# Kernel tuning notes

Measured on AMD Instinct MI355X. Metric: run time of the kernel, lower is better.

The kernel has to match this reference:

```python
import jax, jax.numpy as jnp
import numpy as np
from jax import lax

B, L, D, H = 2, 4096, 1024, 16
K = 4            # short conv kernel size
HD = D // H      # head dim = 64
EPS = 1e-5


def causal_dw_conv(x, w):
    # depthwise causal conv: x [B,L,D], w [D,K]
    xp = jnp.pad(x, ((0, 0), (K - 1, 0), (0, 0)))
    out = xp[:, 0:L, :] * w[:, 0]
    for j in range(1, K):
        out = out + xp[:, j:j + L, :] * w[:, j]
    return out


def setup_inputs() -> dict:
    key = jax.random.key(0)
    ks = jax.random.split(key, 10)
    s = 0.02
    return {
        "hidden_states": jax.random.normal(ks[0], (B, L, D), jnp.float32),
        "Wq": jax.random.normal(ks[1], (D, D), jnp.float32) * s,
        "Wk": jax.random.normal(ks[2], (D, D), jnp.float32) * s,
        "Wv": jax.random.normal(ks[3], (D, D), jnp.float32) * s,
        "Wb": jax.random.normal(ks[4], (D, H), jnp.float32) * s,
        "conv_q": jax.random.normal(ks[5], (D, K), jnp.float32) * s,
        "conv_k": jax.random.normal(ks[6], (D, K), jnp.float32) * s,
        "conv_v": jax.random.normal(ks[7], (D, K), jnp.float32) * s,
        "o_norm_w": jnp.ones((HD,), jnp.float32),
        "Wo": jax.random.normal(ks[8], (D, D), jnp.float32) * s,
    }


def reference(hidden_states, Wq, Wk, Wv, Wb, conv_q, conv_k, conv_v, o_norm_w, Wo):
    x = hidden_states
    # projections + short causal conv with SiLU (qk_activation == 'silu')
    q = jax.nn.silu(causal_dw_conv(x @ Wq, conv_q))
    k = jax.nn.silu(causal_dw_conv(x @ Wk, conv_k))
    v = jax.nn.silu(causal_dw_conv(x @ Wv, conv_v))

    # [B,L,D] -> [L,B,H,hd] for the time scan
    def to_heads(t):
        return t.reshape(B, L, H, HD).transpose(1, 0, 2, 3)

    q, k, v = to_heads(q), to_heads(k), to_heads(v)

    # l2 qk-norm
    q = q / jnp.linalg.norm(q, axis=-1, keepdims=True)
    k = k / jnp.linalg.norm(k, axis=-1, keepdims=True)

    # beta gate [L,B,H]
    beta = jax.nn.sigmoid(x @ Wb).transpose(1, 0, 2)

    def step(S, inp):
        qt, kt, vt, bt = inp  # [B,H,hd] x3, [B,H]
        v_old = jnp.einsum('bhk,bhkv->bhv', kt, S)
        delta = (vt - v_old) * bt[..., None]
        S = S + jnp.einsum('bhk,bhv->bhkv', kt, delta)
        ot = jnp.einsum('bhk,bhkv->bhv', qt, S)
        return S, ot

    S0 = jnp.zeros((B, H, HD, HD), x.dtype)
    _, o = lax.scan(step, S0, (q, k, v, beta))  # o: [L,B,H,hd]
    o = o.transpose(1, 0, 2, 3)  # [B,L,H,hd]

    # per-head RMSNorm
    rms = jax.lax.rsqrt(jnp.mean(o * o, axis=-1, keepdims=True) + EPS)
    o = o * rms * o_norm_w

    return o.reshape(B, L, D) @ Wo
```

## Files before the change

kernel.cpp:

```cpp
#include <hip/hip_runtime.h>
#include <hip/hip_bf16.h>
#include <math.h>

#define BB 2
#define LL 4096
#define DD 1024
#define HH 16
#define HDIM 64
#define CC 64
#define NC 64
#define BH 32
#define GG 8
#define GS 8

typedef __attribute__((ext_vector_type(8))) short short8;
typedef __attribute__((ext_vector_type(4))) float f32x4;
typedef unsigned short u16;
typedef unsigned int u32;

__device__ __forceinline__ u16 f2bf(float f) {
    unsigned int u = __float_as_uint(f);
    unsigned int r = (u + 0x7fffu + ((u >> 16) & 1u)) >> 16;
    return (u16)r;
}
__device__ __forceinline__ float bf2f(u16 h) {
    return __uint_as_float((unsigned)h << 16);
}
__device__ __forceinline__ void split2(float x, u16& h, u16& l) {
    h = f2bf(x);
    l = f2bf(x - bf2f(h));
}
__device__ __forceinline__ u32 packhl(float x) {
    u16 h, l; split2(x, h, l);
    return (u32)h | ((u32)l << 16);
}
__device__ __forceinline__ float unpackhl(u32 v) {
    return bf2f((u16)v) + bf2f((u16)(v >> 16));
}
__device__ __forceinline__ float4 ld_bf4(const u16* p) {
    uint2 v = *(const uint2*)p;
    return make_float4(bf2f((u16)v.x), bf2f((u16)(v.x >> 16)),
                       bf2f((u16)v.y), bf2f((u16)(v.y >> 16)));
}

__device__ __forceinline__ void gld_lds16(const void* g, void* l) {
    __builtin_amdgcn_global_load_lds(
        (const __attribute__((address_space(1))) void*)g,
        (__attribute__((address_space(3))) void*)l, 16, 0, 0);
}

__device__ __forceinline__ int swz(int r, int c) {
    return (r << 6) + ((((c >> 2) ^ (r >> 2)) & 15) << 2) + (c & 3);
}
__device__ __forceinline__ int swze(int r, int c) {
    return (r << 6) + (c ^ (((r ^ (r >> 3)) & 7) << 3));
}

__device__ __forceinline__ void mm64(const u16* __restrict__ Ah, const u16* __restrict__ Al,
                                     const u16* __restrict__ Bh, const u16* __restrict__ Bl,
                                     f32x4* acc, int w, int lane) {
    const int ln = lane & 15, kg = (lane >> 4) * 8;
#pragma unroll
    for (int kb = 0; kb < 2; ++kb) {
        const int k0 = kb * 32 + kg;
        short8 ah = *(const short8*)&Ah[swze(w * 16 + ln, k0)];
        short8 al = *(const short8*)&Al[swze(w * 16 + ln, k0)];
#pragma unroll
        for (int j = 0; j < 4; ++j) {
            short8 bh = *(const short8*)&Bh[swze(j * 16 + ln, k0)];
            short8 bl = *(const short8*)&Bl[swze(j * 16 + ln, k0)];
            acc[j] = __builtin_amdgcn_mfma_f32_16x16x32_bf16(ah, bh, acc[j], 0, 0, 0);
            acc[j] = __builtin_amdgcn_mfma_f32_16x16x32_bf16(ah, bl, acc[j], 0, 0, 0);
            acc[j] = __builtin_amdgcn_mfma_f32_16x16x32_bf16(al, bh, acc[j], 0, 0, 0);
        }
    }
}
__device__ __forceinline__ void mm64_bb(const u16* __restrict__ Ah,
                                        const u16* __restrict__ Bh,
                                        f32x4* acc, int w, int lane) {
    const int ln = lane & 15, kg = (lane >> 4) * 8;
#pragma unroll
    for (int kb = 0; kb < 2; ++kb) {
        const int k0 = kb * 32 + kg;
        short8 ah = *(const short8*)&Ah[swze(w * 16 + ln, k0)];
#pragma unroll
        for (int j = 0; j < 4; ++j) {
            short8 bh = *(const short8*)&Bh[swze(j * 16 + ln, k0)];
            acc[j] = __builtin_amdgcn_mfma_f32_16x16x32_bf16(ah, bh, acc[j], 0, 0, 0);
        }
    }
}
__device__ __forceinline__ void mm64_ab(const u16* __restrict__ Ah,
                                        const u16* __restrict__ Bh, const u16* __restrict__ Bl,
                                        f32x4* acc, int w, int lane) {
    const int ln = lane & 15, kg = (lane >> 4) * 8;
#pragma unroll
    for (int kb = 0; kb < 2; ++kb) {
        const int k0 = kb * 32 + kg;
        short8 ah = *(const short8*)&Ah[swze(w * 16 + ln, k0)];
#pragma unroll
        for (int j = 0; j < 4; ++j) {
            short8 bh = *(const short8*)&Bh[swze(j * 16 + ln, k0)];
            short8 bl = *(const short8*)&Bl[swze(j * 16 + ln, k0)];
            acc[j] = __builtin_amdgcn_mfma_f32_16x16x32_bf16(ah, bh, acc[j], 0, 0, 0);
            acc[j] = __builtin_amdgcn_mfma_f32_16x16x32_bf16(ah, bl, acc[j], 0, 0, 0);
        }
    }
}

__device__ __forceinline__ void g_to_ls(const float* __restrict__ G, u16* Ah, u16* Al, int tid) {
#pragma unroll
    for (int p = 0; p < 4; ++p) {
        int flat = p * 1024 + tid * 4;
        int r = flat >> 6, c = flat & 63;
        float4 v = *(const float4*)&G[flat];
        u16 h0, l0, h1, l1, h2, l2, h3, l3;
        split2(v.x, h0, l0); split2(v.y, h1, l1);
        split2(v.z, h2, l2); split2(v.w, h3, l3);
        int idx = swze(r, c);
        uint2 hv, lv;
        hv.x = (unsigned)h0 | ((unsigned)h1 << 16); hv.y = (unsigned)h2 | ((unsigned)h3 << 16);
        lv.x = (unsigned)l0 | ((unsigned)l1 << 16); lv.y = (unsigned)l2 | ((unsigned)l3 << 16);
        *(uint2*)&Ah[idx] = hv;
        *(uint2*)&Al[idx] = lv;
    }
}
__device__ __forceinline__ void g_to_ls_b(const u16* __restrict__ G16, u16* Ah, int tid) {
#pragma unroll
    for (int p = 0; p < 2; ++p) {
        int flat = p * 2048 + tid * 8;
        int r = flat >> 6, c = flat & 63;
        *(short8*)&Ah[swze(r, c)] = *(const short8*)&G16[flat];
    }
}

__device__ __forceinline__ void pload(uint4 pf[4], const u32* __restrict__ G, int tid) {
    pf[0] = *(const uint4*)&G[tid * 8];
    pf[1] = *(const uint4*)&G[tid * 8 + 4];
    pf[2] = *(const uint4*)&G[2048 + tid * 8];
    pf[3] = *(const uint4*)&G[2048 + tid * 8 + 4];
}
__device__ __forceinline__ void pstore_ls(const uint4 pf[4], u16* Ah, u16* Al, int tid) {
#pragma unroll
    for (int p = 0; p < 2; ++p) {
        int flat = p * 2048 + tid * 8;
        int r = flat >> 6, c = flat & 63;
        uint4 a = pf[2 * p], b = pf[2 * p + 1];
        short8 hi, lo;
        hi[0] = (short)(u16)a.x; hi[1] = (short)(u16)a.y;
        hi[2] = (short)(u16)a.z; hi[3] = (short)(u16)a.w;
        hi[4] = (short)(u16)b.x; hi[5] = (short)(u16)b.y;
        hi[6] = (short)(u16)b.z; hi[7] = (short)(u16)b.w;
        lo[0] = (short)(a.x >> 16); lo[1] = (short)(a.y >> 16);
        lo[2] = (short)(a.z >> 16); lo[3] = (short)(a.w >> 16);
        lo[4] = (short)(b.x >> 16); lo[5] = (short)(b.y >> 16);
        lo[6] = (short)(b.z >> 16); lo[7] = (short)(b.w >> 16);
        *(short8*)&Ah[swze(r, c)] = hi;
        *(short8*)&Al[swze(r, c)] = lo;
    }
}
__device__ __forceinline__ void gp_to_ls(const u32* __restrict__ G, u16* Ah, u16* Al, int tid) {
    uint4 pf[4];
    pload(pf, G, tid);
    pstore_ls(pf, Ah, Al, tid);
}

__device__ __forceinline__ void frag_to_ls(const f32x4* acc, u16* Ah, u16* Al, int w, int lane) {
    const int g = lane >> 4, ln = lane & 15;
#pragma unroll
    for (int j = 0; j < 4; ++j)
#pragma unroll
        for (int r = 0; r < 4; ++r) {
            int row = w * 16 + g * 4 + r, col = j * 16 + ln;
            u16 h, l; split2(acc[j][r], h, l);
            Ah[swze(row, col)] = h;
            Al[swze(row, col)] = l;
        }
}

__device__ __forceinline__ void gp_to_frag(const u32* __restrict__ G, f32x4* acc, int w, int lane) {
    const int g = lane >> 4, ln = lane & 15;
#pragma unroll
    for (int j = 0; j < 4; ++j)
#pragma unroll
        for (int r = 0; r < 4; ++r)
            acc[j][r] = unpackhl(G[(w * 16 + g * 4 + r) * 64 + j * 16 + ln]);
}
__device__ __forceinline__ void gp_add_frag(const u32* __restrict__ G, f32x4* acc, int w, int lane) {
    const int g = lane >> 4, ln = lane & 15;
#pragma unroll
    for (int j = 0; j < 4; ++j)
#pragma unroll
        for (int r = 0; r < 4; ++r)
            acc[j][r] += unpackhl(G[(w * 16 + g * 4 + r) * 64 + j * 16 + ln]);
}
__device__ __forceinline__ void frag_to_gp(const f32x4* acc, u32* __restrict__ G, int w, int lane) {
    const int g = lane >> 4, ln = lane & 15;
#pragma unroll
    for (int j = 0; j < 4; ++j)
#pragma unroll
        for (int r = 0; r < 4; ++r)
            G[(w * 16 + g * 4 + r) * 64 + j * 16 + ln] = packhl(acc[j][r]);
}

__global__ __launch_bounds__(256) void cast_bf16_k(const float* __restrict__ in,
                                                   u16* __restrict__ out) {
    int i = (blockIdx.x * 256 + threadIdx.x) * 8;
    float4 a = *(const float4*)&in[i];
    float4 b = *(const float4*)&in[i + 4];
    uint4 o;
    o.x = (unsigned)f2bf(a.x) | ((unsigned)f2bf(a.y) << 16);
    o.y = (unsigned)f2bf(a.z) | ((unsigned)f2bf(a.w) << 16);
    o.z = (unsigned)f2bf(b.x) | ((unsigned)f2bf(b.y) << 16);
    o.w = (unsigned)f2bf(b.z) | ((unsigned)f2bf(b.w) << 16);
    *(uint4*)&out[i] = o;
}

__global__ __launch_bounds__(256) void transW4_k(const float* __restrict__ W0,
                                                 const float* __restrict__ W1,
                                                 const float* __restrict__ W2,
                                                 const float* __restrict__ W3,
                                                 u16* __restrict__ WT0) {
    __shared__ float t[32][33];
    const int which = blockIdx.z;
    const float* W = (which == 0) ? W0 : (which == 1) ? W1 : (which == 2) ? W2 : W3;
    u16* WT = WT0 + (size_t)which * 1048576;
    const int bx = blockIdx.x * 32, by = blockIdx.y * 32;
#pragma unroll
    for (int p = 0; p < 4; ++p) {
        int idx = p * 256 + threadIdx.x;
        int r = idx >> 5, cc = idx & 31;
        t[r][cc] = W[(size_t)(by + r) * 1024 + bx + cc];
    }
    __syncthreads();
#pragma unroll
    for (int p = 0; p < 4; ++p) {
        int idx = p * 256 + threadIdx.x;
        int r = idx >> 5, cc = idx & 31;
        WT[(size_t)(bx + r) * 1024 + by + cc] = f2bf(t[cc][r]);
    }
}

__device__ __forceinline__ void gemm_core(const u16* A, const u16* BT,
                                          int m0, int n0, f32x4 acc[4][4]) {
    __shared__ __align__(16) short As[3][128 * 32];
    __shared__ __align__(16) short Bs[3][128 * 32];
    const int tid = threadIdx.x;
    const int lane = tid & 63, w = tid >> 6;
    const int wr = w >> 1, wc = w & 1;
    const int ln15 = lane & 15;
    const int erow = tid >> 2;
    const int ecol = (((tid & 3) ^ ((erow >> 1) & 3)) << 3);
    const int kch = lane >> 4;

#define STAGE(buf, k0)                                                        \
    {                                                                         \
        _Pragma("unroll")                                                     \
        for (int r = 0; r < 2; ++r) {                                         \
            gld_lds16(A  + (size_t)(m0 + erow + r * 64) * 1024 + (k0) + ecol, \
                      (short*)As[buf] + r * 2048 + tid * 8);                  \
            gld_lds16(BT + (size_t)(n0 + erow + r * 64) * 1024 + (k0) + ecol, \
                      (short*)Bs[buf] + r * 2048 + tid * 8);                  \
        }                                                                     \
    }

#define COMPUTE(buf)                                                           \
    {                                                                          \
        short8 af[4], bf[4];                                                   \
        _Pragma("unroll")                                                      \
        for (int i = 0; i < 4; ++i) {                                          \
            int row = wr * 64 + i * 16 + ln15;                                 \
            af[i] = *(const short8*)&As[buf][row * 32 + ((kch ^ ((row >> 1) & 3)) << 3)]; \
        }                                                                      \
        _Pragma("unroll")                                                      \
        for (int j = 0; j < 4; ++j) {                                          \
            int row = wc * 64 + j * 16 + ln15;                                 \
            bf[j] = *(const short8*)&Bs[buf][row * 32 + ((kch ^ ((row >> 1) & 3)) << 3)]; \
        }                                                                      \
        __builtin_amdgcn_s_setprio(1);                                         \
        _Pragma("unroll")                                                      \
        for (int i = 0; i < 4; ++i)                                            \
            _Pragma("unroll")                                                  \
            for (int j = 0; j < 4; ++j)                                        \
                acc[i][j] = __builtin_amdgcn_mfma_f32_16x16x32_bf16(af[i], bf[j], acc[i][j], 0, 0, 0); \
        __builtin_amdgcn_s_setprio(0);                                         \
    }

    STAGE(0, 0);
    STAGE(1, 32);
    for (int t = 0; t < 30; ++t) {
        STAGE((t + 2) % 3, (t + 2) * 32);
        asm volatile("s_waitcnt vmcnt(8)" ::: "memory");
        __builtin_amdgcn_sched_barrier(0);
        __builtin_amdgcn_s_barrier();
        COMPUTE(t % 3);
        asm volatile("s_waitcnt lgkmcnt(0)" ::: "memory");
        __builtin_amdgcn_sched_barrier(0);
        __builtin_amdgcn_s_barrier();
    }
    asm volatile("s_waitcnt vmcnt(4)" ::: "memory");
    __builtin_amdgcn_sched_barrier(0);
    __builtin_amdgcn_s_barrier();
    COMPUTE(0);
    asm volatile("s_waitcnt vmcnt(0)" ::: "memory");
    __builtin_amdgcn_sched_barrier(0);
    __builtin_amdgcn_s_barrier();
    COMPUTE(1);
#undef STAGE
#undef COMPUTE
}

__global__ __launch_bounds__(256) void gemm_bf16(const u16* __restrict__ A,
                                                 const u16* __restrict__ BT,
                                                 float* __restrict__ C) {
    const int m0 = blockIdx.y * 128, n0 = blockIdx.x * 128;
    f32x4 acc[4][4] = {};
    gemm_core(A, BT, m0, n0, acc);
    const int lane = threadIdx.x & 63, w = threadIdx.x >> 6;
    const int crow0 = m0 + (w >> 1) * 64 + (lane >> 4) * 4;
    const int ccol0 = n0 + (w & 1) * 64 + (lane & 15);
#pragma unroll
    for (int i = 0; i < 4; ++i)
#pragma unroll
        for (int j = 0; j < 4; ++j)
#pragma unroll
            for (int r = 0; r < 4; ++r)
                C[(size_t)(crow0 + i * 16 + r) * 1024 + ccol0 + j * 16] = acc[i][j][r];
}

__global__ __launch_bounds__(256) void gemm_qkv(const u16* __restrict__ A,
                                                const u16* __restrict__ WT0,
                                                u16* __restrict__ xq16,
                                                u16* __restrict__ xk16,
                                                float* __restrict__ xv) {
    const int which = blockIdx.x >> 3;
    const int n0 = (blockIdx.x & 7) * 128;
    const int m0 = blockIdx.y * 128;
    const u16* BT = WT0 + (size_t)which * 1048576;
    f32x4 acc[4][4] = {};
    gemm_core(A, BT, m0, n0, acc);
    const int lane = threadIdx.x & 63, w = threadIdx.x >> 6;
    const int crow0 = m0 + (w >> 1) * 64 + (lane >> 4) * 4;
    const int ccol0 = n0 + (w & 1) * 64 + (lane & 15);
    if (which == 2) {
#pragma unroll
        for (int i = 0; i < 4; ++i)
#pragma unroll
            for (int j = 0; j < 4; ++j)
#pragma unroll
                for (int r = 0; r < 4; ++r)
                    xv[(size_t)(crow0 + i * 16 + r) * 1024 + ccol0 + j * 16] = acc[i][j][r];
    } else {
        u16* C16 = (which == 0) ? xq16 : xk16;
#pragma unroll
        for (int i = 0; i < 4; ++i)
#pragma unroll
            for (int j = 0; j < 4; ++j)
#pragma unroll
                for (int r = 0; r < 4; ++r)
                    C16[(size_t)(crow0 + i * 16 + r) * 1024 + ccol0 + j * 16] = f2bf(acc[i][j][r]);
    }
}

__global__ __launch_bounds__(256) void beta_k(const float* __restrict__ X,
                                              const float* __restrict__ Wb,
                                              float* __restrict__ beta) {
    int idx = blockIdx.x * 256 + threadIdx.x;
    int row = idx >> 4, h = idx & 15;
    const float* xr = X + (size_t)row * DD;
    float s = 0.f;
    for (int k4 = 0; k4 < DD; k4 += 4) {
        float4 xv = *(const float4*)&xr[k4];
        s += xv.x * Wb[(k4 + 0) * HH + h];
        s += xv.y * Wb[(k4 + 1) * HH + h];
        s += xv.z * Wb[(k4 + 2) * HH + h];
        s += xv.w * Wb[(k4 + 3) * HH + h];
    }
    float bv = 1.f / (1.f + expf(-s));
    int b = row >> 12, l = row & (LL - 1);
    beta[((size_t)b * HH + h) * LL + l] = bv;
}

__global__ __launch_bounds__(256) void conv3_k(const u16* __restrict__ xq16,
                                               const u16* __restrict__ xk16,
                                               const float* __restrict__ xv,
                                               const float* __restrict__ cwq,
                                               const float* __restrict__ cwk,
                                               const float* __restrict__ cwv,
                                               u16* __restrict__ q16,
                                               u16* __restrict__ k16,
                                               float* __restrict__ vout) {
    const int which = blockIdx.z;
    const float* cw = (which == 0) ? cwq : (which == 1) ? cwk : cwv;
    const int l0 = blockIdx.x * 16, b = blockIdx.y;
    const int tid = threadIdx.x;
    const int d0 = tid * 4;
    const float4 w0 = *(const float4*)&cw[(d0 + 0) * 4];
    const float4 w1 = *(const float4*)&cw[(d0 + 1) * 4];
    const float4 w2 = *(const float4*)&cw[(d0 + 2) * 4];
    const float4 w3 = *(const float4*)&cw[(d0 + 3) * 4];
    const int h = d0 >> 6, hd = d0 & 63;
    if (which < 2) {
        const u16* Xb = ((which == 0) ? xq16 : xk16) + (size_t)b * LL * DD;
        u16* O16 = (which == 0) ? q16 : k16;
        float4 xm3 = make_float4(0, 0, 0, 0), xm2 = xm3, xm1 = xm3;
        if (l0 > 0) {
            xm3 = ld_bf4(&Xb[(size_t)(l0 - 3) * DD + d0]);
            xm2 = ld_bf4(&Xb[(size_t)(l0 - 2) * DD + d0]);
            xm1 = ld_bf4(&Xb[(size_t)(l0 - 1) * DD + d0]);
        }
#pragma unroll
        for (int t = 0; t < 16; ++t) {
            const int l = l0 + t;
            float4 xc = ld_bf4(&Xb[(size_t)l * DD + d0]);
            float a0 = xm3.x * w0.x + xm2.x * w0.y + xm1.x * w0.z + xc.x * w0.w;
            float a1 = xm3.y * w1.x + xm2.y * w1.y + xm1.y * w1.z + xc.y * w1.w;
            float a2 = xm3.z * w2.x + xm2.z * w2.y + xm1.z * w2.z + xc.z * w2.w;
            float a3 = xm3.w * w3.x + xm2.w * w3.y + xm1.w * w3.z + xc.w * w3.w;
            a0 = a0 / (1.f + expf(-a0));
            a1 = a1 / (1.f + expf(-a1));
            a2 = a2 / (1.f + expf(-a2));
            a3 = a3 / (1.f + expf(-a3));
            float s = a0 * a0 + a1 * a1 + a2 * a2 + a3 * a3;
            s += __shfl_xor(s, 1);
            s += __shfl_xor(s, 2);
            s += __shfl_xor(s, 4);
            s += __shfl_xor(s, 8);
            float sc = rsqrtf(s);
            a0 *= sc; a1 *= sc; a2 *= sc; a3 *= sc;
            uint2 o;
            o.x = (unsigned)f2bf(a0) | ((unsigned)f2bf(a1) << 16);
            o.y = (unsigned)f2bf(a2) | ((unsigned)f2bf(a3) << 16);
            *(uint2*)&O16[(((size_t)b * HH + h) * LL + l) * 64 + hd] = o;
            xm3 = xm2; xm2 = xm1; xm1 = xc;
        }
    } else {
        const float* Xb = xv + (size_t)b * LL * DD;
        float4 xm3 = make_float4(0, 0, 0, 0), xm2 = xm3, xm1 = xm3;
        if (l0 > 0) {
            xm3 = *(const float4*)&Xb[(size_t)(l0 - 3) * DD + d0];
            xm2 = *(const float4*)&Xb[(size_t)(l0 - 2) * DD + d0];
            xm1 = *(const float4*)&Xb[(size_t)(l0 - 1) * DD + d0];
        }
#pragma unroll
        for (int t = 0; t < 16; ++t) {
            const int l = l0 + t;
            float4 xc = *(const float4*)&Xb[(size_t)l * DD + d0];
            float a0 = xm3.x * w0.x + xm2.x * w0.y + xm1.x * w0.z + xc.x * w0.w;
            float a1 = xm3.y * w1.x + xm2.y * w1.y + xm1.y * w1.z + xc.y * w1.w;
            float a2 = xm3.z * w2.x + xm2.z * w2.y + xm1.z * w2.z + xc.z * w2.w;
            float a3 = xm3.w * w3.x + xm2.w * w3.y + xm1.w * w3.z + xc.w * w3.w;
            a0 = a0 / (1.f + expf(-a0));
            a1 = a1 / (1.f + expf(-a1));
            a2 = a2 / (1.f + expf(-a2));
            a3 = a3 / (1.f + expf(-a3));
            *(float4*)&vout[(((size_t)b * HH + h) * LL + l) * 64 + hd] =
                make_float4(a0, a1, a2, a3);
            xm3 = xm2; xm2 = xm1; xm1 = xc;
        }
    }
}

__global__ __launch_bounds__(256) void phaseA6(const u16* __restrict__ kg16,
                                               const float* __restrict__ vg,
                                               const float* __restrict__ betag,
                                               u32* __restrict__ WgP,
                                               u32* __restrict__ UgTP,
                                               u32* __restrict__ PallP,
                                               u32* __restrict__ BallTP) {
    __shared__ __align__(16) char pool[73728];
    u16* Kh   = (u16*)pool;
    u16* KTh  = (u16*)(pool + 8192);
    float* At = (float*)(pool + 16384);
    float* WU = (float*)(pool + 32768);
    u16* WTh  = (u16*)pool;
    u16* WTl  = (u16*)(pool + 16384);
    u16* UTh  = (u16*)(pool + 24576);
    u16* UTl  = (u16*)(pool + 65536);
    float* scr = (float*)(pool + 32768);

    const int c = blockIdx.x, bh = blockIdx.y;
    const int tid = threadIdx.x, lane = tid & 63, w = tid >> 6;
    const int g = lane >> 4, ln = lane & 15;
    const int t0 = (tid >> 4) * 4, d4 = (tid & 15) * 4;
    const size_t base = ((size_t)bh * LL + (size_t)c * 64) * 64;
    const size_t obase = ((size_t)bh * NC + c) * 4096;
    const float* bet = betag + (size_t)bh * LL + (size_t)c * 64;

    g_to_ls_b(kg16 + base, Kh, tid);
    {
        u16 kv[4][4];
#pragma unroll
        for (int i = 0; i < 4; ++i) {
            uint2 v = *(const uint2*)&kg16[base + (size_t)(t0 + i) * 64 + d4];
            kv[i][0] = (u16)v.x; kv[i][1] = (u16)(v.x >> 16);
            kv[i][2] = (u16)v.y; kv[i][3] = (u16)(v.y >> 16);
        }
#pragma unroll
        for (int j = 0; j < 4; ++j) {
            uint2 hv;
            hv.x = (unsigned)kv[0][j] | ((unsigned)kv[1][j] << 16);
            hv.y = (unsigned)kv[2][j] | ((unsigned)kv[3][j] << 16);
            *(uint2*)&KTh[swze(d4 + j, t0)] = hv;
        }
    }
    __syncthreads();
    {
        f32x4 acc[4] = {};
        mm64_bb(Kh, Kh, acc, w, lane);
#pragma unroll
        for (int r = 0; r < 4; ++r) {
            int t = w * 16 + g * 4 + r;
            float bt = bet[t];
#pragma unroll
            for (int j = 0; j < 4; ++j) {
                int s = j * 16 + ln;
                At[t * 64 + s] = (s < t) ? bt * acc[j][r] : 0.f;
            }
        }
    }
#pragma unroll
    for (int p = 0; p < 8; ++p) {
        int flat = p * 1024 + tid * 4;
        int t = flat >> 7, j = flat & 127;
        float bt = bet[t];
        float4 src;
        if (j < 64) src = ld_bf4(&Kh[swze(t, j)]);
        else        src = *(const float4*)&vg[base + (size_t)t * 64 + (j - 64)];
        src.x *= bt; src.y *= bt; src.z *= bt; src.w *= bt;
        *(float4*)&WU[t * 128 + j] = src;
    }
    __syncthreads();
#pragma unroll
    for (int pb = 0; pb < 4; ++pb) {
        const int r0 = pb * 16;
        if (pb > 0) {
            const int col = tid & 127;
            const int rbase = r0 + (tid >> 7) * 8;
            float acc8[8] = {};
            for (int r = 0; r < r0; r += 4) {
                float u0 = WU[(r + 0) * 128 + col], u1 = WU[(r + 1) * 128 + col];
                float u2 = WU[(r + 2) * 128 + col], u3 = WU[(r + 3) * 128 + col];
#pragma unroll
                for (int i = 0; i < 8; ++i) {
                    float4 a4 = *(const float4*)&At[(rbase + i) * 64 + r];
                    acc8[i] += a4.x * u0 + a4.y * u1 + a4.z * u2 + a4.w * u3;
                }
            }
#pragma unroll
            for (int i = 0; i < 8; ++i) WU[(rbase + i) * 128 + col] -= acc8[i];
            __syncthreads();
        }
        if (tid < 128) {
            const int col = tid;
            float wv[16];
            wv[0] = WU[r0 * 128 + col];
#pragma unroll
            for (int t = 1; t < 16; ++t) {
                float a = WU[(r0 + t) * 128 + col];
#pragma unroll
                for (int r = 0; r < t; ++r) a -= At[(r0 + t) * 64 + r0 + r] * wv[r];
                wv[t] = a;
            }
#pragma unroll
            for (int t = 1; t < 16; ++t) WU[(r0 + t) * 128 + col] = wv[t];
        }
        __syncthreads();
    }
#pragma unroll
    for (int p = 0; p < 4; ++p) {
        int flat = p * 1024 + tid * 4;
        int t = flat >> 6, j = flat & 63;
        float4 v = *(const float4*)&WU[t * 128 + j];
        uint4 o;
        o.x = packhl(v.x); o.y = packhl(v.y); o.z = packhl(v.z); o.w = packhl(v.w);
        *(uint4*)&WgP[obase + flat] = o;
    }
    {
        u16 h4[4][4], l4[4][4];
#pragma unroll
        for (int i = 0; i < 4; ++i) {
            float4 v = *(const float4*)&WU[(t0 + i) * 128 + d4];
            split2(v.x, h4[i][0], l4[i][0]); split2(v.y, h4[i][1], l4[i][1]);
            split2(v.z, h4[i][2], l4[i][2]); split2(v.w, h4[i][3], l4[i][3]);
        }
#pragma unroll
        for (int j = 0; j < 4; ++j) {
            uint2 hv, lv;
            hv.x = (unsigned)h4[0][j] | ((unsigned)h4[1][j] << 16);
            hv.y = (unsigned)h4[2][j] | ((unsigned)h4[3][j] << 16);
            lv.x = (unsigned)l4[0][j] | ((unsigned)l4[1][j] << 16);
            lv.y = (unsigned)l4[2][j] | ((unsigned)l4[3][j] << 16);
            *(uint2*)&WTh[swze(d4 + j, t0)] = hv;
            *(uint2*)&WTl[swze(d4 + j, t0)] = lv;
        }
#pragma unroll
        for (int i = 0; i < 4; ++i) {
            float4 v = *(const float4*)&WU[(t0 + i) * 128 + 64 + d4];
            split2(v.x, h4[i][0], l4[i][0]); split2(v.y, h4[i][1], l4[i][1]);
            split2(v.z, h4[i][2], l4[i][2]); split2(v.w, h4[i][3], l4[i][3]);
        }
#pragma unroll
        for (int j = 0; j < 4; ++j) {
            uint2 hv, lv;
            hv.x = (unsigned)h4[0][j] | ((unsigned)h4[1][j] << 16);
            hv.y = (unsigned)h4[2][j] | ((unsigned)h4[3][j] << 16);
            lv.x = (unsigned)l4[0][j] | ((unsigned)l4[1][j] << 16);
            lv.y = (unsigned)l4[2][j] | ((unsigned)l4[3][j] << 16);
            *(uint2*)&UTh[swze(d4 + j, t0)] = hv;
            *(uint2*)&UTl[swze(d4 + j, t0)] = lv;
        }
    }
    __syncthreads();
#pragma unroll
    for (int p = 0; p < 4; ++p) {
        int flat = p * 1024 + tid * 4;
        int n = flat >> 6, tt = flat & 63;
        int idx = swze(n, tt);
        uint2 hh = *(const uint2*)&UTh[idx];
        uint2 ll2 = *(const uint2*)&UTl[idx];
        uint4 o;
        o.x = (hh.x & 0xffffu) | (ll2.x << 16);
        o.y = (hh.x >> 16) | (ll2.x & 0xffff0000u);
        o.z = (hh.y & 0xffffu) | (ll2.y << 16);
        o.w = (hh.y >> 16) | (ll2.y & 0xffff0000u);
        *(uint4*)&UgTP[obase + flat] = o;
    }
    f32x4 aP[4] = {}, aB[4] = {};
    mm64_ab(KTh, WTh, WTl, aP, w, lane);
    mm64_ab(KTh, UTh, UTl, aB, w, lane);
#pragma unroll
    for (int j = 0; j < 4; ++j)
#pragma unroll
        for (int r = 0; r < 4; ++r) {
            int row = w * 16 + g * 4 + r, col = j * 16 + ln;
            float pv = ((row == col) ? 1.f : 0.f) - aP[j][r];
            PallP[obase + (size_t)row * 64 + col] = packhl(pv);
            scr[swz(row, col)] = aB[j][r];
        }
    __syncthreads();
#pragma unroll
    for (int p = 0; p < 4; ++p) {
        int flat = p * 1024 + tid * 4;
        int n = flat >> 6, dd = flat & 63;
        uint4 o;
        o.x = packhl(scr[swz(dd + 0, n)]);
        o.y = packhl(scr[swz(dd + 1, n)]);
        o.z = packhl(scr[swz(dd + 2, n)]);
        o.w = packhl(scr[swz(dd + 3, n)]);
        *(uint4*)&BallTP[obase + flat] = o;
    }
}

__global__ __launch_bounds__(256) void compose4(const u32* __restrict__ PallP,
                                                const u32* __restrict__ BallTP,
                                                u32* __restrict__ PgP,
                                                u32* __restrict__ BgTP) {
    __shared__ __align__(16) char pool[81920];
    u16* Ph = (u16*)pool;
    u16* Pl = (u16*)(pool + 8192);
    u16* Bh = (u16*)(pool + 16384);
    u16* Bl = (u16*)(pool + 24576);
    u16* nh = (u16*)(pool + 32768);
    u16* nl = (u16*)(pool + 40960);
    float* scr = (float*)(pool + 49152);
    const int g = blockIdx.x, bh = blockIdx.y;
    const int tid = threadIdx.x, lane = tid & 63, w = tid >> 6;
    const int gi = lane >> 4, ln = lane & 15;
    const size_t base0 = ((size_t)bh * NC + (size_t)g * GS) * 4096;
    f32x4 mP[4], mB[4];
#pragma unroll
    for (int p = 0; p < 4; ++p) {
        int flat = p * 1024 + tid * 4;
        int r = flat >> 6, c4 = flat & 63;
        uint4 pk = *(const uint4*)&PallP[base0 + flat];
        *(float4*)&scr[swz(r, c4)] =
            make_float4(unpackhl(pk.x), unpackhl(pk.y), unpackhl(pk.z), unpackhl(pk.w));
    }
    gp_to_frag(BallTP + base0, mB, w, lane);
    __syncthreads();
#pragma unroll
    for (int j = 0; j < 4; ++j)
#pragma unroll
        for (int r = 0; r < 4; ++r) {
            int row = w * 16 + gi * 4 + r, col = j * 16 + ln;
            mP[j][r] = scr[swz(col, row)];
        }
    uint4 pf[4];
    pload(pf, PallP + base0 + 4096, tid);
    for (int s = 1; s < GS; ++s) {
        __syncthreads();
        frag_to_ls(mP, Ph, Pl, w, lane);
        frag_to_ls(mB, Bh, Bl, w, lane);
        pstore_ls(pf, nh, nl, tid);
        __syncthreads();
        if (s < GS - 1) pload(pf, PallP + base0 + (size_t)(s + 1) * 4096, tid);
        f32x4 aP[4] = {}, aB[4] = {};
        mm64(Ph, Pl, nh, nl, aP, w, lane);
        mm64(Bh, Bl, nh, nl, aB, w, lane);
        gp_add_frag(BallTP + base0 + (size_t)s * 4096, aB, w, lane);
#pragma unroll
        for (int j = 0; j < 4; ++j) { mP[j] = aP[j]; mB[j] = aB[j]; }
    }
    const size_t gbase = ((size_t)bh * GG + g) * 4096;
    frag_to_gp(mB, BgTP + gbase, w, lane);
    __syncthreads();
#pragma unroll
    for (int j = 0; j < 4; ++j)
#pragma unroll
        for (int r = 0; r < 4; ++r) {
            int row = w * 16 + gi * 4 + r, col = j * 16 + ln;
            scr[swz(row, col)] = mP[j][r];
        }
    __syncthreads();
#pragma unroll
    for (int p = 0; p < 4; ++p) {
        int flat = p * 1024 + tid * 4;
        int a = flat >> 6, b0 = flat & 63;
        uint4 o;
        o.x = packhl(scr[swz(b0 + 0, a)]);
        o.y = packhl(scr[swz(b0 + 1, a)]);
        o.z = packhl(scr[swz(b0 + 2, a)]);
        o.w = packhl(scr[swz(b0 + 3, a)]);
        *(uint4*)&PgP[gbase + flat] = o;
    }
}

__global__ __launch_bounds__(256) void scanG4(const u32* __restrict__ PgP,
                                              const u32* __restrict__ BgTP,
                                              u32* __restrict__ SallTP) {
    __shared__ __align__(16) char pool[32768];
    u16* Sh = (u16*)pool;
    u16* Sl = (u16*)(pool + 8192);
    u16* nh = (u16*)(pool + 16384);
    u16* nl = (u16*)(pool + 24576);
    const int bh = blockIdx.x;
    const int tid = threadIdx.x, lane = tid & 63, w = tid >> 6;
    f32x4 mS[4] = {};
    for (int g = 0; g < GG; ++g) {
        const size_t sbase = ((size_t)bh * NC + (size_t)g * GS) * 4096;
        frag_to_gp(mS, SallTP + sbase, w, lane);
        if (g == GG - 1) break;
        __syncthreads();
        frag_to_ls(mS, Sh, Sl, w, lane);
        gp_to_ls(PgP + ((size_t)bh * GG + g) * 4096, nh, nl, tid);
        __syncthreads();
        f32x4 a[4] = {};
        mm64(Sh, Sl, nh, nl, a, w, lane);
        gp_add_frag(BgTP + ((size_t)bh * GG + g) * 4096, a, w, lane);
#pragma unroll
        for (int j = 0; j < 4; ++j) mS[j] = a[j];
    }
}

__global__ __launch_bounds__(256) void rollout4(const u32* __restrict__ PallP,
                                                const u32* __restrict__ BallTP,
                                                u32* __restrict__ SallTP) {
    __shared__ __align__(16) char pool[32768];
    u16* Sh = (u16*)pool;
    u16* Sl = (u16*)(pool + 8192);
    u16* nh = (u16*)(pool + 16384);
    u16* nl = (u16*)(pool + 24576);
    const int g = blockIdx.x, bh = blockIdx.y;
    const int tid = threadIdx.x, lane = tid & 63, w = tid >> 6;
    const size_t base0 = ((size_t)bh * NC + (size_t)g * GS) * 4096;
    f32x4 mS[4];
    gp_to_frag(SallTP + base0, mS, w, lane);
    uint4 pf[4];
    pload(pf, PallP + base0, tid);
    for (int j = 1; j < GS; ++j) {
        __syncthreads();
        frag_to_ls(mS, Sh, Sl, w, lane);
        pstore_ls(pf, nh, nl, tid);
        __syncthreads();
        if (j < GS - 1) pload(pf, PallP + base0 + (size_t)j * 4096, tid);
        f32x4 a[4] = {};
        mm64(Sh, Sl, nh, nl, a, w, lane);
        gp_add_frag(BallTP + base0 + (size_t)(j - 1) * 4096, a, w, lane);
#pragma unroll
        for (int jj = 0; jj < 4; ++jj) mS[jj] = a[jj];
        frag_to_gp(mS, SallTP + base0 + (size_t)j * 4096, w, lane);
    }
}

__global__ __launch_bounds__(256) void phaseO5(const u32* __restrict__ WgP,
                                               const u32* __restrict__ UgTP,
                                               const u16* __restrict__ qg16,
                                               const u16* __restrict__ kg16,
                                               const u32* __restrict__ SallTP,
                                               const float* __restrict__ nw,
                                               u16* __restrict__ ob) {
    __shared__ __align__(16) char pool[57344];
    u16* Qh = (u16*)pool;
    u16* Kh = (u16*)(pool + 8192);
    u16* Wh = (u16*)(pool + 16384);
    u16* Wl = (u16*)(pool + 24576);
    u16* Sh = (u16*)(pool + 32768);
    u16* Sl = (u16*)(pool + 40960);
    u16* Dl = (u16*)(pool + 49152);
    u16* Dh = Kh;
    u16* Mh = Wh; u16* Ml = Wl;
    const int c = blockIdx.x, bh = blockIdx.y;
    const int b = bh >> 4, h = bh & 15;
    const int tid = threadIdx.x, lane = tid & 63, w = tid >> 6;
    const int gi = lane >> 4, ln = lane & 15;
    const size_t tbase = ((size_t)bh * NC + c) * 4096;
    const size_t qkbase = ((size_t)bh * LL + (size_t)c * 64) * 64;
    g_to_ls_b(qg16 + qkbase, Qh, tid);
    g_to_ls_b(kg16 + qkbase, Kh, tid);
    gp_to_ls(WgP + tbase, Wh, Wl, tid);
    gp_to_ls(SallTP + tbase, Sh, Sl, tid);
    __syncthreads();
    f32x4 aM[4] = {}, aD[4] = {};
    mm64_bb(Qh, Kh, aM, w, lane);
    mm64(Sh, Sl, Wh, Wl, aD, w, lane);
    __syncthreads();
#pragma unroll
    for (int j = 0; j < 4; ++j)
#pragma unroll
        for (int r = 0; r < 4; ++r) {
            int row = w * 16 + gi * 4 + r, col = j * 16 + ln;
            float mv = (col <= row) ? aM[j][r] : 0.f;
            u16 mh_, ml_; split2(mv, mh_, ml_);
            Mh[swze(row, col)] = mh_;
            Ml[swze(row, col)] = ml_;
            float dv = unpackhl(UgTP[tbase + (size_t)row * 64 + col]) - aD[j][r];
            u16 dh_, dl_; split2(dv, dh_, dl_);
            Dh[swze(row, col)] = dh_;
            Dl[swze(row, col)] = dl_;
        }
    __syncthreads();
    f32x4 aO[4] = {};
    mm64_ab(Qh, Sh, Sl, aO, w, lane);
    mm64(Mh, Ml, Dh, Dl, aO, w, lane);
    float nwv[4];
#pragma unroll
    for (int j = 0; j < 4; ++j) nwv[j] = nw[j * 16 + ln];
#pragma unroll
    for (int r = 0; r < 4; ++r) {
        float ss = 0.f;
#pragma unroll
        for (int j = 0; j < 4; ++j) ss += aO[j][r] * aO[j][r];
        ss += __shfl_xor(ss, 1);
        ss += __shfl_xor(ss, 2);
        ss += __shfl_xor(ss, 4);
        ss += __shfl_xor(ss, 8);
        float rms = rsqrtf(ss * (1.f / 64.f) + 1e-5f);
        int row = w * 16 + gi * 4 + r;
        size_t orow = ((size_t)b * LL + (size_t)c * 64 + row) * DD + (size_t)h * 64;
#pragma unroll
        for (int j = 0; j < 4; ++j)
            ob[orow + j * 16 + ln] = f2bf(aO[j][r] * rms * nwv[j]);
    }
}

extern "C" void kernel_launch(void* const* d_in, const int* in_sizes, int n_in,
                              void* d_out, int out_size, void* d_ws, size_t ws_size,
                              hipStream_t stream) {
    const float* x  = (const float*)d_in[0];
    const float* Wq = (const float*)d_in[1];
    const float* Wk = (const float*)d_in[2];
    const float* Wv = (const float*)d_in[3];
    const float* Wb = (const float*)d_in[4];
    const float* cq = (const float*)d_in[5];
    const float* ck = (const float*)d_in[6];
    const float* cv = (const float*)d_in[7];
    const float* nw = (const float*)d_in[8];
    const float* Wo = (const float*)d_in[9];
    float* out = (float*)d_out;
    float* ws = (float*)d_ws;

    const size_t SZ = (size_t)BB * LL * DD;
    float* xv    = ws;
    float* v     = ws + SZ;
    u32* WgP     = (u32*)(ws + 2 * SZ);
    u32* UgTP    = (u32*)(ws + 3 * SZ);
    u32* SallTP  = (u32*)(ws + 4 * SZ);
    u16* xb   = (u16*)(ws + 5 * SZ);
    u16* q16  = xb;
    u16* xq16 = (u16*)(ws + 5 * SZ) + SZ;
    u16* xk16 = (u16*)(ws + 5 * SZ) + 2 * SZ;
    u16* k16  = (u16*)(ws + 5 * SZ) + 3 * SZ;
    float* beta = ws + 7 * SZ;
    u16* wqT  = (u16*)(beta + (size_t)BH * LL);
    u32* PgP  = (u32*)(wqT + (size_t)4 * 1048576);
    u32* BgTP = PgP + 1048576;

    u32* PallP  = (u32*)xv;
    u32* BallTP = (u32*)out;
    u16* ob   = (u16*)v;
    u16* woT  = wqT + (size_t)3 * 1048576;

    dim3 blk(256);

    cast_bf16_k<<<dim3(4096), blk, 0, stream>>>(x, xb);
    transW4_k<<<dim3(32, 32, 4), blk, 0, stream>>>(Wq, Wk, Wv, Wo, wqT);
    gemm_qkv<<<dim3(24, 64), blk, 0, stream>>>(xb, wqT, xq16, xk16, xv);
    beta_k<<<dim3(512), blk, 0, stream>>>(x, Wb, beta);
    conv3_k<<<dim3(LL / 16, BB, 3), blk, 0, stream>>>(xq16, xk16, xv, cq, ck, cv, q16, k16, v);
    phaseA6<<<dim3(NC, BH), blk, 0, stream>>>(k16, v, beta, WgP, UgTP, PallP, BallTP);
    compose4<<<dim3(GG, BH), blk, 0, stream>>>(PallP, BallTP, PgP, BgTP);
    scanG4<<<dim3(BH), blk, 0, stream>>>(PgP, BgTP, SallTP);
    rollout4<<<dim3(GG, BH), blk, 0, stream>>>(PallP, BallTP, SallTP);
    phaseO5<<<dim3(NC, BH), blk, 0, stream>>>(WgP, UgTP, q16, k16, SallTP, nw, ob);
    gemm_bf16<<<dim3(8, 64), blk, 0, stream>>>(ob, woT, out);
}
```

Baseline: 362.9 us.

## Enlarge GEMM tiles to 256x256 with 512 threads and register double-buffered fragments

Replaces the 128x128, 256-thread GEMM core with a 256x256 tile computed by 8 waves. It uses a 4-deep LDS ring and ping-pongs A/B fragments in registers, so LDS reads for the next k-step overlap the current MFMAs. The aim is more data reuse per loaded byte and fewer barrier stalls in the QKV and output projections. In exchange, the grids shrink: the output GEMM becomes 128 blocks, fewer than the CU count. The 128 KB of LDS plus the large accumulator set also limit occupancy.

```diff
diff --git a/kernel.cpp b/kernel.cpp
--- a/kernel.cpp
+++ b/kernel.cpp
@@ -241,86 +241,86 @@
     }
 }
 
-__device__ __forceinline__ void gemm_core(const u16* A, const u16* BT,
-                                          int m0, int n0, f32x4 acc[4][4]) {
-    __shared__ __align__(16) short As[3][128 * 32];
-    __shared__ __align__(16) short Bs[3][128 * 32];
+__device__ __forceinline__ void gemm_core256(const u16* A, const u16* BT,
+                                             int m0, int n0, f32x4 acc[8][4]) {
+    __shared__ __align__(16) short As[4][256 * 32];
+    __shared__ __align__(16) short Bs[4][256 * 32];
     const int tid = threadIdx.x;
     const int lane = tid & 63, w = tid >> 6;
-    const int wr = w >> 1, wc = w & 1;
-    const int ln15 = lane & 15;
+    const int wr = w >> 2, wc = w & 3;
+    const int ln15 = lane & 15, kch = lane >> 4;
     const int erow = tid >> 2;
-    const int ecol = (((tid & 3) ^ ((erow >> 1) & 3)) << 3);
-    const int kch = lane >> 4;
-
-#define STAGE(buf, k0)                                                        \
-    {                                                                         \
+    const int ecol = (((tid & 3) ^ ((tid >> 3) & 3)) << 3);
+
+#define STAGE256(buf, t)                                                      \
+    {   const int k0_ = (t) * 32;                                             \
         _Pragma("unroll")                                                     \
-        for (int r = 0; r < 2; ++r) {                                         \
-            gld_lds16(A  + (size_t)(m0 + erow + r * 64) * 1024 + (k0) + ecol, \
-                      (short*)As[buf] + r * 2048 + tid * 8);                  \
-            gld_lds16(BT + (size_t)(n0 + erow + r * 64) * 1024 + (k0) + ecol, \
-                      (short*)Bs[buf] + r * 2048 + tid * 8);                  \
+        for (int rr = 0; rr < 2; ++rr) {                                      \
+            gld_lds16(A  + (size_t)(m0 + rr * 128 + erow) * 1024 + k0_ + ecol,\
+                      (short*)As[buf] + rr * 4096 + tid * 8);                 \
+            gld_lds16(BT + (size_t)(n0 + rr * 128 + erow) * 1024 + k0_ + ecol,\
+                      (short*)Bs[buf] + rr * 4096 + tid * 8);                 \
+        } }
+
+#define RF256(Fa, Fb, buf)                                                    \
+    {   _Pragma("unroll")                                                     \
+        for (int i = 0; i < 8; ++i) {                                         \
+            int row = wr * 128 + i * 16 + ln15;                               \
+            Fa[i] = *(const short8*)&As[buf][row * 32 + ((kch ^ ((row >> 1) & 3)) << 3)]; \
         }                                                                     \
-    }
-
-#define COMPUTE(buf)                                                           \
-    {                                                                          \
-        short8 af[4], bf[4];                                                   \
-        _Pragma("unroll")                                                      \
-        for (int i = 0; i < 4; ++i) {                                          \
-            int row = wr * 64 + i * 16 + ln15;                                 \
-            af[i] = *(const short8*)&As[buf][row * 32 + ((kch ^ ((row >> 1) & 3)) << 3)]; \
-        }                                                                      \
-        _Pragma("unroll")                                                      \
-        for (int j = 0; j < 4; ++j) {                                          \
-            int row = wc * 64 + j * 16 + ln15;                                 \
-            bf[j] = *(const short8*)&Bs[buf][row * 32 + ((kch ^ ((row >> 1) & 3)) << 3)]; \
-        }                                                                      \
-        __builtin_amdgcn_s_setprio(1);                                         \
-        _Pragma("unroll")                                                      \
-        for (int i = 0; i < 4; ++i)                                            \
-            _Pragma("unroll")                                                  \
-            for (int j = 0; j < 4; ++j)                                        \
-                acc[i][j] = __builtin_amdgcn_mfma_f32_16x16x32_bf16(af[i], bf[j], acc[i][j], 0, 0, 0); \
-        __builtin_amdgcn_s_setprio(0);                                         \
-    }
-
-    STAGE(0, 0);
-    STAGE(1, 32);
-    for (int t = 0; t < 30; ++t) {
-        STAGE((t + 2) % 3, (t + 2) * 32);
-        asm volatile("s_waitcnt vmcnt(8)" ::: "memory");
-        __builtin_amdgcn_sched_barrier(0);
-        __builtin_amdgcn_s_barrier();
-        COMPUTE(t % 3);
-        asm volatile("s_waitcnt lgkmcnt(0)" ::: "memory");
-        __builtin_amdgcn_sched_barrier(0);
-        __builtin_amdgcn_s_barrier();
-    }
-    asm volatile("s_waitcnt vmcnt(4)" ::: "memory");
-    __builtin_amdgcn_sched_barrier(0);
+        _Pragma("unroll")                                                     \
+        for (int j = 0; j < 4; ++j) {                                         \
+            int row = wc * 64 + j * 16 + ln15;                                \
+            Fb[j] = *(const short8*)&Bs[buf][row * 32 + ((kch ^ ((row >> 1) & 3)) << 3)]; \
+        } }
+
+#define MM256(Fa, Fb)                                                         \
+    {   __builtin_amdgcn_s_setprio(1);                                        \
+        _Pragma("unroll")                                                     \
+        for (int i = 0; i < 8; ++i)                                           \
+            _Pragma("unroll")                                                 \
+            for (int j = 0; j < 4; ++j)                                       \
+                acc[i][j] = __builtin_amdgcn_mfma_f32_16x16x32_bf16(Fa[i], Fb[j], acc[i][j], 0, 0, 0); \
+        __builtin_amdgcn_s_setprio(0); }
+
+#define BODY256(t, Ca, Cb, Na, Nb)                                            \
+    {   if ((t) + 3 < 32) STAGE256(((t) + 3) & 3, (t) + 3);                   \
+        if ((t) < 29)       asm volatile("s_waitcnt vmcnt(8)" ::: "memory");  \
+        else if ((t) == 29) asm volatile("s_waitcnt vmcnt(4)" ::: "memory");  \
+        else if ((t) == 30) asm volatile("s_waitcnt vmcnt(0)" ::: "memory");  \
+        asm volatile("s_waitcnt lgkmcnt(0)" ::: "memory");                    \
+        __builtin_amdgcn_s_barrier();                                         \
+        if ((t) < 31) RF256(Na, Nb, ((t) + 1) & 3);                           \
+        MM256(Ca, Cb); }
+
+    short8 Xa[8], Xb[4], Ya[8], Yb[4];
+    STAGE256(0, 0);
+    STAGE256(1, 1);
+    STAGE256(2, 2);
+    asm volatile("s_waitcnt vmcnt(8)" ::: "memory");
     __builtin_amdgcn_s_barrier();
-    COMPUTE(0);
-    asm volatile("s_waitcnt vmcnt(0)" ::: "memory");
-    __builtin_amdgcn_sched_barrier(0);
-    __builtin_amdgcn_s_barrier();
-    COMPUTE(1);
-#undef STAGE
-#undef COMPUTE
-}
-
-__global__ __launch_bounds__(256) void gemm_bf16(const u16* __restrict__ A,
-                                                 const u16* __restrict__ BT,
-                                                 float* __restrict__ C) {
-    const int m0 = blockIdx.y * 128, n0 = blockIdx.x * 128;
-    f32x4 acc[4][4] = {};
-    gemm_core(A, BT, m0, n0, acc);
+    RF256(Xa, Xb, 0);
+    for (int t2 = 0; t2 < 32; t2 += 2) {
+        BODY256(t2, Xa, Xb, Ya, Yb);
+        BODY256(t2 + 1, Ya, Yb, Xa, Xb);
+    }
+#undef STAGE256
+#undef RF256
+#undef MM256
+#undef BODY256
+}
+
+__global__ __launch_bounds__(512, 2) void gemm_bf16(const u16* __restrict__ A,
+                                                    const u16* __restrict__ BT,
+                                                    float* __restrict__ C) {
+    const int m0 = blockIdx.y * 256, n0 = blockIdx.x * 256;
+    f32x4 acc[8][4] = {};
+    gemm_core256(A, BT, m0, n0, acc);
     const int lane = threadIdx.x & 63, w = threadIdx.x >> 6;
-    const int crow0 = m0 + (w >> 1) * 64 + (lane >> 4) * 4;
-    const int ccol0 = n0 + (w & 1) * 64 + (lane & 15);
-#pragma unroll
-    for (int i = 0; i < 4; ++i)
+    const int crow0 = m0 + (w >> 2) * 128 + (lane >> 4) * 4;
+    const int ccol0 = n0 + (w & 3) * 64 + (lane & 15);
+#pragma unroll
+    for (int i = 0; i < 8; ++i)
 #pragma unroll
         for (int j = 0; j < 4; ++j)
 #pragma unroll
@@ -328,23 +328,23 @@
                 C[(size_t)(crow0 + i * 16 + r) * 1024 + ccol0 + j * 16] = acc[i][j][r];
 }
 
-__global__ __launch_bounds__(256) void gemm_qkv(const u16* __restrict__ A,
-                                                const u16* __restrict__ WT0,
-                                                u16* __restrict__ xq16,
-                                                u16* __restrict__ xk16,
-                                                float* __restrict__ xv) {
-    const int which = blockIdx.x >> 3;
-    const int n0 = (blockIdx.x & 7) * 128;
-    const int m0 = blockIdx.y * 128;
+__global__ __launch_bounds__(512, 2) void gemm_qkv(const u16* __restrict__ A,
+                                                   const u16* __restrict__ WT0,
+                                                   u16* __restrict__ xq16,
+                                                   u16* __restrict__ xk16,
+                                                   float* __restrict__ xv) {
+    const int which = blockIdx.x >> 2;
+    const int n0 = (blockIdx.x & 3) * 256;
+    const int m0 = blockIdx.y * 256;
     const u16* BT = WT0 + (size_t)which * 1048576;
-    f32x4 acc[4][4] = {};
-    gemm_core(A, BT, m0, n0, acc);
+    f32x4 acc[8][4] = {};
+    gemm_core256(A, BT, m0, n0, acc);
     const int lane = threadIdx.x & 63, w = threadIdx.x >> 6;
-    const int crow0 = m0 + (w >> 1) * 64 + (lane >> 4) * 4;
-    const int ccol0 = n0 + (w & 1) * 64 + (lane & 15);
+    const int crow0 = m0 + (w >> 2) * 128 + (lane >> 4) * 4;
+    const int ccol0 = n0 + (w & 3) * 64 + (lane & 15);
     if (which == 2) {
 #pragma unroll
-        for (int i = 0; i < 4; ++i)
+        for (int i = 0; i < 8; ++i)
 #pragma unroll
             for (int j = 0; j < 4; ++j)
 #pragma unroll
@@ -353,7 +353,7 @@
     } else {
         u16* C16 = (which == 0) ? xq16 : xk16;
 #pragma unroll
-        for (int i = 0; i < 4; ++i)
+        for (int i = 0; i < 8; ++i)
 #pragma unroll
             for (int j = 0; j < 4; ++j)
 #pragma unroll
@@ -895,7 +895,7 @@
 
     cast_bf16_k<<<dim3(4096), blk, 0, stream>>>(x, xb);
     transW4_k<<<dim3(32, 32, 4), blk, 0, stream>>>(Wq, Wk, Wv, Wo, wqT);
-    gemm_qkv<<<dim3(24, 64), blk, 0, stream>>>(xb, wqT, xq16, xk16, xv);
+    gemm_qkv<<<dim3(12, 32), dim3(512), 0, stream>>>(xb, wqT, xq16, xk16, xv);
     beta_k<<<dim3(512), blk, 0, stream>>>(x, Wb, beta);
     conv3_k<<<dim3(LL / 16, BB, 3), blk, 0, stream>>>(xq16, xk16, xv, cq, ck, cv, q16, k16, v);
     phaseA6<<<dim3(NC, BH), blk, 0, stream>>>(k16, v, beta, WgP, UgTP, PallP, BallTP);
@@ -903,5 +903,5 @@
     scanG4<<<dim3(BH), blk, 0, stream>>>(PgP, BgTP, SallTP);
     rollout4<<<dim3(GG, BH), blk, 0, stream>>>(PallP, BallTP, SallTP);
     phaseO5<<<dim3(NC, BH), blk, 0, stream>>>(WgP, UgTP, q16, k16, SallTP, nw, ob);
-    gemm_bf16<<<dim3(8, 64), blk, 0, stream>>>(ob, woT, out);
-}
+    gemm_bf16<<<dim3(4, 32), dim3(512), 0, stream>>>(ob, woT, out);
+}
```

Result: faster. 355.6 us (-2.0%).
